# Kernel tuning notes

Hardware: AMD Instinct MI355X
Metric: run time of the kernel (lower is better)

The kernel has to match this reference:

```python
import jax, jax.numpy as jnp
import numpy as np

B, T, N, F_IN, F_OUT, K = 16, 12, 1024, 64, 64, 3


def setup_inputs() -> dict:
    key = jax.random.key(0)
    k1, k2, k3, k4 = jax.random.split(key, 4)
    x = jax.random.normal(k1, (B, T, N, F_IN), dtype=jnp.float32)
    spatial_attention = jax.random.uniform(k2, (B, N, N), dtype=jnp.float32)
    cheb = jax.random.normal(k3, (K, N, N), dtype=jnp.float32) / np.sqrt(N)
    # Xavier-uniform-ish init for Theta [K, F_in, F_out]
    limit = np.sqrt(6.0 / (F_IN + F_OUT))
    Theta = jax.random.uniform(k4, (K, F_IN, F_OUT), dtype=jnp.float32,
                               minval=-limit, maxval=limit)
    return {"x": x, "spatial_attention": spatial_attention, "cheb": cheb, "Theta": Theta}


def reference(x, spatial_attention, cheb, Theta):
    # Attention-weighted Chebyshev adjacencies: [B, K, N, N]
    A = cheb[None, :, :, :] * spatial_attention[:, None, :, :]
    # Graph propagation for all t, k at once: [B, T, K, N, F_in]
    rhs = jnp.einsum('bkij,btjf->btkif', A, x)
    # Per-order linear map + sum over K: [B, T, N, F_out]
    out = jnp.einsum('btkif,kfo->btio', rhs, Theta)
    return jax.nn.relu(out)
```

## Files before the change

### kernel.cpp

```cpp
#include <hip/hip_runtime.h>
#include <hip/hip_bf16.h>

#define BB 16
#define TT 12
#define NN 1024
#define FF 64
#define KC 3

typedef __bf16  bf16x8 __attribute__((ext_vector_type(8)));
typedef float   f32x4  __attribute__((ext_vector_type(4)));
typedef float   f32x16 __attribute__((ext_vector_type(16)));
typedef unsigned short u16;

#define A_TILE 24576
#define MFMA_B(a, b, c) __builtin_amdgcn_mfma_f32_32x32x16_bf16(a, b, c, 0, 0, 0)

#define YF_BYTES 25165824ull
#define CB_BYTES 6291456ull

static __device__ __forceinline__ u16 f2bf(float v) {
    union { __bf16 b; u16 u; } c; c.b = (__bf16)v; return c.u;
}

__global__ __launch_bounds__(256) void x_to_yfrags(
    const float* __restrict__ x, u16* __restrict__ y)
{
    __shared__ char tl[64 * 128];
    const int tid = threadIdx.x;
    const int bt  = blockIdx.x >> 4;
    const int jt  = blockIdx.x & 15;
    const int f   = tid & 63;
    const int jr  = tid >> 6;

    const float* xp = x + ((size_t)bt * NN + jt * 64 + jr) * FF + f;
    #pragma unroll
    for (int stp = 0; stp < 16; ++stp) {
        int j = stp * 4 + jr;
        u16 h = f2bf(xp[stp * 4 * FF]);
        *reinterpret_cast<u16*>(tl + j * 128 + ((f * 2) ^ ((j & 7) << 4))) = h;
    }
    __syncthreads();

    u16* yo = y + ((size_t)bt * 16 + jt) * 4096;
    #pragma unroll
    for (int p = 0; p < 2; ++p) {
        int c  = tid + p * 256;
        int s  = c >> 6, fo = c & 63;
        int j0 = (s >> 1) * 16 + (s & 1) * 8;
        u16 h[8];
        #pragma unroll
        for (int e = 0; e < 8; ++e)
            h[e] = *reinterpret_cast<u16*>(tl + (j0 + e) * 128 + ((fo * 2) ^ (e << 4)));
        uint4 w;
        w.x = h[0] | ((unsigned)h[1] << 16);
        w.y = h[2] | ((unsigned)h[3] << 16);
        w.z = h[4] | ((unsigned)h[5] << 16);
        w.w = h[6] | ((unsigned)h[7] << 16);
        *reinterpret_cast<uint4*>(yo + (size_t)c * 8) = w;
    }
}

__global__ __launch_bounds__(256) void cheb_to_bf16(
    const float* __restrict__ c, u16* __restrict__ o)
{
    const size_t i = ((size_t)blockIdx.x * 256 + threadIdx.x) * 8;
    f32x4 a = *reinterpret_cast<const f32x4*>(c + i);
    f32x4 b = *reinterpret_cast<const f32x4*>(c + i + 4);
    u16 h[8];
    #pragma unroll
    for (int e = 0; e < 4; ++e) { h[e] = f2bf(a[e]); h[e + 4] = f2bf(b[e]); }
    uint4 w;
    w.x = h[0] | ((unsigned)h[1] << 16);
    w.y = h[2] | ((unsigned)h[3] << 16);
    w.z = h[4] | ((unsigned)h[5] << 16);
    w.w = h[6] | ((unsigned)h[7] << 16);
    *reinterpret_cast<uint4*>(o + i) = w;
}

__global__ __launch_bounds__(512, 1) void cheb_main(
    const u16*  __restrict__ yfr,
    const float* __restrict__ att,
    const u16*  __restrict__ chb,
    const float* __restrict__ Theta,
    float* __restrict__ out)
{
    __shared__ __align__(16) char lds[2 * A_TILE];
    char* Ab0 = lds;
    char* Ab1 = lds + A_TILE;

    const int tid  = threadIdx.x;
    const int lane = tid & 63;
    const int wid  = tid >> 6;

    const int wg = (blockIdx.x & 7) * 96 + (blockIdx.x >> 3);
    const int b  = wg / 48;
    const int it = (wg % 48) / 3;
    const int tc = wg % 3;
    const int i_base = it * 64;
    const int t_base = tc * 4;

    const int wm  = wid >> 1;
    const int wn  = wid & 1;
    const int l31 = lane & 31;
    const int lg  = lane >> 5;
    const int sw3 = (l31 >> 2) & 7;

    const int r_a = tid >> 3;
    const int g_a = tid & 7;
    const int swza_st = ((r_a >> 2) & 7) << 4;
    const float* attR = att + ((size_t)b * NN + i_base + r_a) * NN + g_a * 8;
    const u16*   chR  = chb + ((size_t)(i_base + r_a)) * NN + g_a * 8;

    const u16* yt0 = yfr + ((size_t)(b * TT + t_base + wm) * 16) * 4096
                   + (size_t)(lg * 512 + l31 * 8);

    f32x16 acc[KC][2] = {};
    const int arow = (wn * 32 + l31) * 128;

    f32x4 ra0, ra1;
    bf16x8 rc[KC];
    bf16x8 y0[8], y1[8];

    auto LOADS = [&](int j0) {
        ra0 = *reinterpret_cast<const f32x4*>(attR + j0);
        ra1 = *reinterpret_cast<const f32x4*>(attR + j0 + 4);
        #pragma unroll
        for (int k = 0; k < KC; ++k)
            rc[k] = *reinterpret_cast<const bf16x8*>(chR + (size_t)k * NN * NN + j0);
    };
    auto FINISH = [&](char* Ab) {
        #pragma unroll
        for (int k = 0; k < KC; ++k) {
            bf16x8 w;
            #pragma unroll
            for (int e = 0; e < 4; ++e) {
                w[e]     = (__bf16)(ra0[e] * (float)rc[k][e]);
                w[e + 4] = (__bf16)(ra1[e] * (float)rc[k][e + 4]);
            }
            *reinterpret_cast<bf16x8*>(
                Ab + (k * 64 + r_a) * 128 + ((g_a * 16) ^ swza_st)) = w;
        }
    };
    auto loadY = [&](bf16x8* yd, int jt) {
        const u16* yt = yt0 + (size_t)jt * 4096;
        #pragma unroll
        for (int q = 0; q < 4; ++q) {
            yd[q * 2]     = *reinterpret_cast<const bf16x8*>(yt + q * 1024);
            yd[q * 2 + 1] = *reinterpret_cast<const bf16x8*>(yt + q * 1024 + 256);
        }
    };

    auto phase = [&](const char* AbR, bf16x8 af0, bf16x8 af1, int kk) {
        const int off = ((kk * 2 + lg) ^ sw3) << 4;
        bf16x8 b0 = *reinterpret_cast<const bf16x8*>(AbR + arow + off);
        bf16x8 b1 = *reinterpret_cast<const bf16x8*>(AbR + 8192 + arow + off);
        bf16x8 b2 = *reinterpret_cast<const bf16x8*>(AbR + 16384 + arow + off);
        __builtin_amdgcn_s_setprio(1);
        acc[0][0] = MFMA_B(af0, b0, acc[0][0]); acc[0][1] = MFMA_B(af1, b0, acc[0][1]);
        acc[1][0] = MFMA_B(af0, b1, acc[1][0]); acc[1][1] = MFMA_B(af1, b1, acc[1][1]);
        acc[2][0] = MFMA_B(af0, b2, acc[2][0]); acc[2][1] = MFMA_B(af1, b2, acc[2][1]);
        __builtin_amdgcn_s_setprio(0);
    };

    auto body = [&](char* curAb, char* altAb, bf16x8* yC, bf16x8* yN, int jt) {
        loadY(yN, (jt + 1) & 15);
        phase(curAb, yC[0], yC[1], 0);
        phase(curAb, yC[2], yC[3], 1);
        phase(curAb, yC[4], yC[5], 2);
        phase(curAb, yC[6], yC[7], 3);
        if (jt < 15) {
            FINISH(altAb);
            LOADS(((jt + 2) & 15) * 64);
        }
        asm volatile("s_waitcnt lgkmcnt(0)" ::: "memory");
        __builtin_amdgcn_s_barrier();
    };

    LOADS(0);
    loadY(y0, 0);
    FINISH(Ab0);
    LOADS(64);
    asm volatile("s_waitcnt lgkmcnt(0)" ::: "memory");
    __builtin_amdgcn_s_barrier();

    #pragma unroll 1
    for (int jt2 = 0; jt2 < 8; ++jt2) {
        body(Ab0, Ab1, y0, y1, jt2 * 2);
        body(Ab1, Ab0, y1, y0, jt2 * 2 + 1);
    }

    {
        const int fi0 = wid * 3;
        #pragma unroll
        for (int q = 0; q < 3; ++q) {
            int fi = fi0 + q;
            int k  = fi >> 3;
            int mo = (fi >> 2) & 1;
            int s  = fi & 3;
            int o  = 32 * mo + l31;
            int fb = 32 * (s >> 1) + 16 * (s & 1) + 4 * lg;
            bf16x8 v;
            #pragma unroll
            for (int e = 0; e < 8; ++e) {
                int f = fb + (e & 3) + 8 * (e >> 2);
                v[e] = (__bf16)Theta[(k * FF + f) * FF + o];
            }
            *reinterpret_cast<bf16x8*>(lds + (fi * 64 + lane) * 16) = v;
        }
    }
    __syncthreads();

    f32x16 of[2] = {};
    #pragma unroll
    for (int k = 0; k < KC; ++k) {
        #pragma unroll
        for (int s = 0; s < 4; ++s) {
            bf16x8 pb;
            #pragma unroll
            for (int e = 0; e < 8; ++e)
                pb[e] = (__bf16)acc[k][s >> 1][e + 8 * (s & 1)];
            #pragma unroll
            for (int mo = 0; mo < 2; ++mo) {
                bf16x8 th = *reinterpret_cast<const bf16x8*>(
                    lds + ((((k * 2 + mo) * 4 + s) * 64) + lane) * 16);
                of[mo] = MFMA_B(pb, th, of[mo]);
            }
        }
    }

    const int t = t_base + wm;
    float* op = out + (((size_t)b * TT + t) * NN + i_base + wn * 32) * FF;
    #pragma unroll
    for (int mo = 0; mo < 2; ++mo) {
        #pragma unroll
        for (int r = 0; r < 16; ++r) {
            int row = (r & 3) + 8 * (r >> 2) + 4 * lg;
            int o   = 32 * mo + l31;
            float v = of[mo][r];
            op[(size_t)row * FF + o] = v > 0.0f ? v : 0.0f;
        }
    }
}

__global__ __launch_bounds__(512, 2) void cheb_fused(
    const float* __restrict__ x, const float* __restrict__ att,
    const float* __restrict__ cheb, const float* __restrict__ Theta,
    float* __restrict__ out)
{
    __shared__ __align__(16) char lds_raw[2 * (A_TILE + 32768)];
    char* Ab0 = lds_raw;
    char* Xb0 = lds_raw + A_TILE;
    char* Ab1 = lds_raw + A_TILE + 32768;
    char* Xb1 = Ab1 + A_TILE;

    const int tid  = threadIdx.x;
    const int lane = tid & 63;
    const int wid  = tid >> 6;
    const int wg = (blockIdx.x & 7) * 96 + (blockIdx.x >> 3);
    const int b  = wg / 48;
    const int it = (wg % 48) / 3;
    const int tc = wg % 3;
    const int i_base = it * 64;
    const int t_base = tc * 4;
    const int wm  = wid >> 1;
    const int wn  = wid & 1;
    const int l31 = lane & 31;
    const int lg  = lane >> 5;
    const int sw3 = (l31 >> 2) & 7;
    const float* attB = att + (size_t)b * NN * NN;
    const float* xB   = x + (size_t)b * TT * NN * FF;
    const int r_a = tid >> 3;
    const int g_a = tid & 7;
    const int swza_st = ((r_a >> 2) & 7) << 4;
    int tl_s[4], jj_s[4], f_s[4], swzx_st[4];
    #pragma unroll
    for (int s = 0; s < 4; ++s) {
        int u = tid + s * 512;
        tl_s[s] = u >> 9;
        int rem = u & 511;
        jj_s[s] = (rem >> 4) * 2;
        f_s[s]  = (rem & 15) * 4;
        swzx_st[s] = ((f_s[s] >> 2) & 7) << 4;
    }
    f32x4 ra0, ra1, rc0[KC], rc1[KC], rx0[4], rx1[4];
    auto load_tile = [&](int j0) {
        const float* ap = attB + (size_t)(i_base + r_a) * NN + j0 + g_a * 8;
        ra0 = *reinterpret_cast<const f32x4*>(ap);
        ra1 = *reinterpret_cast<const f32x4*>(ap + 4);
        #pragma unroll
        for (int k = 0; k < KC; ++k) {
            const float* cp = cheb + ((size_t)k * NN + i_base + r_a) * NN + j0 + g_a * 8;
            rc0[k] = *reinterpret_cast<const f32x4*>(cp);
            rc1[k] = *reinterpret_cast<const f32x4*>(cp + 4);
        }
        #pragma unroll
        for (int s = 0; s < 4; ++s) {
            const float* xp = xB + ((size_t)(t_base + tl_s[s]) * NN + j0 + jj_s[s]) * FF + f_s[s];
            rx0[s] = *reinterpret_cast<const f32x4*>(xp);
            rx1[s] = *reinterpret_cast<const f32x4*>(xp + FF);
        }
    };
    auto store_A = [&](char* Ab) {
        #pragma unroll
        for (int k = 0; k < KC; ++k) {
            bf16x8 w;
            #pragma unroll
            for (int e = 0; e < 4; ++e) {
                w[e]     = (__bf16)(rc0[k][e] * ra0[e]);
                w[e + 4] = (__bf16)(rc1[k][e] * ra1[e]);
            }
            *reinterpret_cast<bf16x8*>(Ab + (k * 64 + r_a) * 128 + ((g_a * 16) ^ swza_st)) = w;
        }
    };
    auto store_X = [&](char* Xb) {
        #pragma unroll
        for (int s = 0; s < 4; ++s) {
            const int c0 = tl_s[s] * 64 + f_s[s];
            const int coloff = (jj_s[s] * 2) ^ swzx_st[s];
            #pragma unroll
            for (int e = 0; e < 4; ++e) {
                union { __bf16 h[2]; unsigned u32; } pk;
                pk.h[0] = (__bf16)rx0[s][e];
                pk.h[1] = (__bf16)rx1[s][e];
                *reinterpret_cast<unsigned*>(Xb + (c0 + e) * 128 + coloff) = pk.u32;
            }
        }
    };
    f32x16 acc[KC][2] = {};
    const int xrow0 = (wm * 64 + l31) * 128;
    const int xrow1 = xrow0 + 32 * 128;
    const int arow  = (wn * 32 + l31) * 128;
    auto phase = [&](const char* AbR, const char* XbR, int kk) {
        const int off = ((kk * 2 + lg) ^ sw3) << 4;
        bf16x8 af0 = *reinterpret_cast<const bf16x8*>(XbR + xrow0 + off);
        bf16x8 af1 = *reinterpret_cast<const bf16x8*>(XbR + xrow1 + off);
        bf16x8 b0  = *reinterpret_cast<const bf16x8*>(AbR + arow + off);
        bf16x8 b1  = *reinterpret_cast<const bf16x8*>(AbR + 8192 + arow + off);
        bf16x8 b2  = *reinterpret_cast<const bf16x8*>(AbR + 16384 + arow + off);
        __builtin_amdgcn_s_setprio(1);
        acc[0][0] = MFMA_B(af0, b0, acc[0][0]); acc[0][1] = MFMA_B(af1, b0, acc[0][1]);
        acc[1][0] = MFMA_B(af0, b1, acc[1][0]); acc[1][1] = MFMA_B(af1, b1, acc[1][1]);
        acc[2][0] = MFMA_B(af0, b2, acc[2][0]); acc[2][1] = MFMA_B(af1, b2, acc[2][1]);
        __builtin_amdgcn_s_setprio(0);
    };
    load_tile(0);
    store_A(Ab0);
    store_X(Xb0);
    load_tile(64);
    asm volatile("s_waitcnt lgkmcnt(0)" ::: "memory");
    __builtin_amdgcn_s_barrier();
    for (int jt2 = 0; jt2 < 8; ++jt2) {
        const int jt = jt2 * 2;
        phase(Ab0, Xb0, 0);
        phase(Ab0, Xb0, 1);
        store_A(Ab1);
        phase(Ab0, Xb0, 2);
        store_X(Xb1);
        phase(Ab0, Xb0, 3);
        if (jt + 2 < 16) load_tile((jt + 2) * 64);
        asm volatile("s_waitcnt lgkmcnt(0)" ::: "memory");
        __builtin_amdgcn_s_barrier();
        phase(Ab1, Xb1, 0);
        phase(Ab1, Xb1, 1);
        if (jt + 1 < 15) store_A(Ab0);
        phase(Ab1, Xb1, 2);
        if (jt + 1 < 15) store_X(Xb0);
        phase(Ab1, Xb1, 3);
        if (jt + 3 < 16) load_tile((jt + 3) * 64);
        asm volatile("s_waitcnt lgkmcnt(0)" ::: "memory");
        __builtin_amdgcn_s_barrier();
    }
    {
        const int fi0 = wid * 3;
        #pragma unroll
        for (int q = 0; q < 3; ++q) {
            int fi = fi0 + q;
            int k  = fi >> 3;
            int mo = (fi >> 2) & 1;
            int s  = fi & 3;
            int o  = 32 * mo + l31;
            int fb = 32 * (s >> 1) + 16 * (s & 1) + 4 * lg;
            bf16x8 v;
            #pragma unroll
            for (int e = 0; e < 8; ++e) {
                int f = fb + (e & 3) + 8 * (e >> 2);
                v[e] = (__bf16)Theta[(k * FF + f) * FF + o];
            }
            *reinterpret_cast<bf16x8*>(lds_raw + (fi * 64 + lane) * 16) = v;
        }
    }
    __syncthreads();
    f32x16 of[2] = {};
    #pragma unroll
    for (int k = 0; k < KC; ++k) {
        #pragma unroll
        for (int s = 0; s < 4; ++s) {
            bf16x8 pb;
            #pragma unroll
            for (int e = 0; e < 8; ++e)
                pb[e] = (__bf16)acc[k][s >> 1][e + 8 * (s & 1)];
            #pragma unroll
            for (int mo = 0; mo < 2; ++mo) {
                bf16x8 th = *reinterpret_cast<const bf16x8*>(
                    lds_raw + ((((k * 2 + mo) * 4 + s) * 64) + lane) * 16);
                of[mo] = MFMA_B(pb, th, of[mo]);
            }
        }
    }
    const int t = t_base + wm;
    float* op = out + (((size_t)b * TT + t) * NN + i_base + wn * 32) * FF;
    #pragma unroll
    for (int mo = 0; mo < 2; ++mo) {
        #pragma unroll
        for (int r = 0; r < 16; ++r) {
            int row = (r & 3) + 8 * (r >> 2) + 4 * lg;
            int o   = 32 * mo + l31;
            float v = of[mo][r];
            op[(size_t)row * FF + o] = v > 0.0f ? v : 0.0f;
        }
    }
}

extern "C" void kernel_launch(void* const* d_in, const int* in_sizes, int n_in,
                              void* d_out, int out_size, void* d_ws, size_t ws_size,
                              hipStream_t stream) {
    const float* x     = (const float*)d_in[0];
    const float* att   = (const float*)d_in[1];
    const float* cheb  = (const float*)d_in[2];
    const float* Theta = (const float*)d_in[3];
    float* out = (float*)d_out;
    (void)in_sizes; (void)n_in; (void)out_size;

    if (ws_size >= YF_BYTES + CB_BYTES) {
        u16* yfr = (u16*)d_ws;
        u16* cbf = (u16*)((char*)d_ws + YF_BYTES);
        x_to_yfrags<<<dim3(BB * TT * 16), 256, 0, stream>>>(x, yfr);
        cheb_to_bf16<<<dim3(KC * NN * NN / (256 * 8)), 256, 0, stream>>>(cheb, cbf);
        cheb_main<<<dim3(BB * 16 * 3), 512, 0, stream>>>(yfr, att, cbf, Theta, out);
    } else {
        cheb_fused<<<dim3(BB * 16 * 3), 512, 0, stream>>>(x, att, cheb, Theta, out);
    }
}
```

Baseline: 108.7 us.

## Process two j-tiles per barrier interval with paired LDS buffers

Doubles LDS to hold two A tiles per buffer, so each barrier interval computes two j-tiles and builds the next pair. This halves the number of workgroup barriers and moves the A-tile construction (FINISH/LOADS) ahead of the MFMA phases to overlap global loads with compute. In exchange, LDS use grows to 96KB and register pressure rises. The last iterations also build tiles that wrap around modulo 16 and are never used.

```diff
diff --git a/kernel.cpp b/kernel.cpp
--- a/kernel.cpp
+++ b/kernel.cpp
@@ -13,6 +13,7 @@
 typedef unsigned short u16;
 
 #define A_TILE 24576
+#define A_PAIR (2 * A_TILE)
 #define MFMA_B(a, b, c) __builtin_amdgcn_mfma_f32_32x32x16_bf16(a, b, c, 0, 0, 0)
 
 #define YF_BYTES 25165824ull
@@ -84,9 +85,9 @@
     const float* __restrict__ Theta,
     float* __restrict__ out)
 {
-    __shared__ __align__(16) char lds[2 * A_TILE];
+    __shared__ __align__(16) char lds[2 * A_PAIR];
     char* Ab0 = lds;
-    char* Ab1 = lds + A_TILE;
+    char* Ab1 = lds + A_PAIR;
 
     const int tid  = threadIdx.x;
     const int lane = tid & 63;
@@ -150,43 +151,50 @@
         }
     };
 
-    auto phase = [&](const char* AbR, bf16x8 af0, bf16x8 af1, int kk) {
-        const int off = ((kk * 2 + lg) ^ sw3) << 4;
-        bf16x8 b0 = *reinterpret_cast<const bf16x8*>(AbR + arow + off);
-        bf16x8 b1 = *reinterpret_cast<const bf16x8*>(AbR + 8192 + arow + off);
-        bf16x8 b2 = *reinterpret_cast<const bf16x8*>(AbR + 16384 + arow + off);
-        __builtin_amdgcn_s_setprio(1);
-        acc[0][0] = MFMA_B(af0, b0, acc[0][0]); acc[0][1] = MFMA_B(af1, b0, acc[0][1]);
-        acc[1][0] = MFMA_B(af0, b1, acc[1][0]); acc[1][1] = MFMA_B(af1, b1, acc[1][1]);
-        acc[2][0] = MFMA_B(af0, b2, acc[2][0]); acc[2][1] = MFMA_B(af1, b2, acc[2][1]);
-        __builtin_amdgcn_s_setprio(0);
-    };
-
-    auto body = [&](char* curAb, char* altAb, bf16x8* yC, bf16x8* yN, int jt) {
-        loadY(yN, (jt + 1) & 15);
-        phase(curAb, yC[0], yC[1], 0);
-        phase(curAb, yC[2], yC[3], 1);
-        phase(curAb, yC[4], yC[5], 2);
-        phase(curAb, yC[6], yC[7], 3);
-        if (jt < 15) {
-            FINISH(altAb);
-            LOADS(((jt + 2) & 15) * 64);
-        }
+    auto phase4 = [&](const char* Abase, const bf16x8* yv) {
+        #pragma unroll
+        for (int kk = 0; kk < 4; ++kk) {
+            const int off = ((kk * 2 + lg) ^ sw3) << 4;
+            bf16x8 af0 = yv[kk * 2];
+            bf16x8 af1 = yv[kk * 2 + 1];
+            bf16x8 b0 = *reinterpret_cast<const bf16x8*>(Abase + arow + off);
+            bf16x8 b1 = *reinterpret_cast<const bf16x8*>(Abase + 8192 + arow + off);
+            bf16x8 b2 = *reinterpret_cast<const bf16x8*>(Abase + 16384 + arow + off);
+            __builtin_amdgcn_s_setprio(1);
+            acc[0][0] = MFMA_B(af0, b0, acc[0][0]); acc[0][1] = MFMA_B(af1, b0, acc[0][1]);
+            acc[1][0] = MFMA_B(af0, b1, acc[1][0]); acc[1][1] = MFMA_B(af1, b1, acc[1][1]);
+            acc[2][0] = MFMA_B(af0, b2, acc[2][0]); acc[2][1] = MFMA_B(af1, b2, acc[2][1]);
+            __builtin_amdgcn_s_setprio(0);
+        }
+    };
+
+    auto interval = [&](char* cur, char* alt, int p) {
+        loadY(y1, (p + 1) & 15);
+        FINISH(alt);
+        LOADS(((p + 3) & 15) * 64);
+        phase4(cur, y0);
+        loadY(y0, (p + 2) & 15);
+        FINISH(alt + A_TILE);
+        LOADS(((p + 4) & 15) * 64);
+        phase4(cur + A_TILE, y1);
         asm volatile("s_waitcnt lgkmcnt(0)" ::: "memory");
         __builtin_amdgcn_s_barrier();
     };
 
     LOADS(0);
-    loadY(y0, 0);
     FINISH(Ab0);
     LOADS(64);
+    FINISH(Ab0 + A_TILE);
+    LOADS(128);
+    loadY(y0, 0);
     asm volatile("s_waitcnt lgkmcnt(0)" ::: "memory");
     __builtin_amdgcn_s_barrier();
 
     #pragma unroll 1
-    for (int jt2 = 0; jt2 < 8; ++jt2) {
-        body(Ab0, Ab1, y0, y1, jt2 * 2);
-        body(Ab1, Ab0, y1, y0, jt2 * 2 + 1);
+    for (int h = 0; h < 8; ++h) {
+        char* cur = (h & 1) ? Ab1 : Ab0;
+        char* alt = (h & 1) ? Ab0 : Ab1;
+        interval(cur, alt, 2 * h);
     }
 
     {
```

After: 121.2 us. 1.11x slower.

## Stage Y fragments through double-buffered LDS via direct global-to-LDS loads

Applied to the files above, without the earlier changes.

Y operand fragments are no longer prefetched into per-wave register arrays. Each block now loads them once into a double-buffered LDS region with global_load_lds, and every wave reads them from LDS inside the MFMA loop. This removes the duplicate global loads made by waves that share the same Y rows, and frees the 64 VGPRs the y0/y1 arrays used. In exchange it adds LDS reads per k-step, grows shared memory to about 112KB, and depends on a hand-written vmcnt(5) wait for correct ordering.

```diff
diff --git a/kernel.cpp b/kernel.cpp
--- a/kernel.cpp
+++ b/kernel.cpp
@@ -13,6 +13,7 @@
 typedef unsigned short u16;
 
 #define A_TILE 24576
+#define Y_TILE 32768
 #define MFMA_B(a, b, c) __builtin_amdgcn_mfma_f32_32x32x16_bf16(a, b, c, 0, 0, 0)
 
 #define YF_BYTES 25165824ull
@@ -20,6 +21,12 @@
 
 static __device__ __forceinline__ u16 f2bf(float v) {
     union { __bf16 b; u16 u; } c; c.b = (__bf16)v; return c.u;
+}
+
+static __device__ __forceinline__ void load_lds16(const void* g, void* l) {
+    __builtin_amdgcn_global_load_lds(
+        (const __attribute__((address_space(1))) unsigned int*)g,
+        (__attribute__((address_space(3))) unsigned int*)l, 16, 0, 0);
 }
 
 __global__ __launch_bounds__(256) void x_to_yfrags(
@@ -84,9 +91,11 @@
     const float* __restrict__ Theta,
     float* __restrict__ out)
 {
-    __shared__ __align__(16) char lds[2 * A_TILE];
+    __shared__ __align__(16) char lds[2 * A_TILE + 2 * Y_TILE];
     char* Ab0 = lds;
     char* Ab1 = lds + A_TILE;
+    char* Yb0 = lds + 2 * A_TILE;
+    char* Yb1 = Yb0 + Y_TILE;
 
     const int tid  = threadIdx.x;
     const int lane = tid & 63;
@@ -111,15 +120,11 @@
     const float* attR = att + ((size_t)b * NN + i_base + r_a) * NN + g_a * 8;
     const u16*   chR  = chb + ((size_t)(i_base + r_a)) * NN + g_a * 8;
 
-    const u16* yt0 = yfr + ((size_t)(b * TT + t_base + wm) * 16) * 4096
-                   + (size_t)(lg * 512 + l31 * 8);
-
     f32x16 acc[KC][2] = {};
     const int arow = (wn * 32 + l31) * 128;
 
     f32x4 ra0, ra1;
     bf16x8 rc[KC];
-    bf16x8 y0[8], y1[8];
 
     auto LOADS = [&](int j0) {
         ra0 = *reinterpret_cast<const f32x4*>(attR + j0);
@@ -141,52 +146,63 @@
                 Ab + (k * 64 + r_a) * 128 + ((g_a * 16) ^ swza_st)) = w;
         }
     };
-    auto loadY = [&](bf16x8* yd, int jt) {
-        const u16* yt = yt0 + (size_t)jt * 4096;
+
+    auto loadY_lds = [&](char* Yb, int jt) {
         #pragma unroll
         for (int q = 0; q < 4; ++q) {
-            yd[q * 2]     = *reinterpret_cast<const bf16x8*>(yt + q * 1024);
-            yd[q * 2 + 1] = *reinterpret_cast<const bf16x8*>(yt + q * 1024 + 256);
-        }
-    };
-
-    auto phase = [&](const char* AbR, bf16x8 af0, bf16x8 af1, int kk) {
-        const int off = ((kk * 2 + lg) ^ sw3) << 4;
-        bf16x8 b0 = *reinterpret_cast<const bf16x8*>(AbR + arow + off);
-        bf16x8 b1 = *reinterpret_cast<const bf16x8*>(AbR + 8192 + arow + off);
-        bf16x8 b2 = *reinterpret_cast<const bf16x8*>(AbR + 16384 + arow + off);
-        __builtin_amdgcn_s_setprio(1);
-        acc[0][0] = MFMA_B(af0, b0, acc[0][0]); acc[0][1] = MFMA_B(af1, b0, acc[0][1]);
-        acc[1][0] = MFMA_B(af0, b1, acc[1][0]); acc[1][1] = MFMA_B(af1, b1, acc[1][1]);
-        acc[2][0] = MFMA_B(af0, b2, acc[2][0]); acc[2][1] = MFMA_B(af1, b2, acc[2][1]);
-        __builtin_amdgcn_s_setprio(0);
-    };
-
-    auto body = [&](char* curAb, char* altAb, bf16x8* yC, bf16x8* yN, int jt) {
-        loadY(yN, (jt + 1) & 15);
-        phase(curAb, yC[0], yC[1], 0);
-        phase(curAb, yC[2], yC[3], 1);
-        phase(curAb, yC[4], yC[5], 2);
-        phase(curAb, yC[6], yC[7], 3);
+            int s    = wid * 4 + q;
+            int tile = s >> 3;
+            int part = s & 7;
+            const u16* gp = yfr + ((size_t)(b * TT + t_base + tile) * 16 + jt) * 4096
+                          + (size_t)(part * 64 + lane) * 8;
+            load_lds16(gp, Yb + tile * 8192 + part * 1024);
+        }
+    };
+
+    auto phase4 = [&](const char* Abase, const char* Ybase) {
+        const char* yt = Ybase + wm * 8192;
+        #pragma unroll
+        for (int kk = 0; kk < 4; ++kk) {
+            const int off  = ((kk * 2 + lg) ^ sw3) << 4;
+            const int yoff = (kk * 2 + lg) * 1024 + l31 * 16;
+            bf16x8 af0 = *reinterpret_cast<const bf16x8*>(yt + yoff);
+            bf16x8 af1 = *reinterpret_cast<const bf16x8*>(yt + yoff + 512);
+            bf16x8 b0 = *reinterpret_cast<const bf16x8*>(Abase + arow + off);
+            bf16x8 b1 = *reinterpret_cast<const bf16x8*>(Abase + 8192 + arow + off);
+            bf16x8 b2 = *reinterpret_cast<const bf16x8*>(Abase + 16384 + arow + off);
+            __builtin_amdgcn_s_setprio(1);
+            acc[0][0] = MFMA_B(af0, b0, acc[0][0]); acc[0][1] = MFMA_B(af1, b0, acc[0][1]);
+            acc[1][0] = MFMA_B(af0, b1, acc[1][0]); acc[1][1] = MFMA_B(af1, b1, acc[1][1]);
+            acc[2][0] = MFMA_B(af0, b2, acc[2][0]); acc[2][1] = MFMA_B(af1, b2, acc[2][1]);
+            __builtin_amdgcn_s_setprio(0);
+        }
+    };
+
+    auto body = [&](char* curA, char* altA, char* curY, char* altY, int jt) {
+        loadY_lds(altY, (jt + 1) & 15);
+        __builtin_amdgcn_sched_barrier(0);
+        phase4(curA, curY);
         if (jt < 15) {
-            FINISH(altAb);
+            FINISH(altA);
             LOADS(((jt + 2) & 15) * 64);
         }
+        asm volatile("s_waitcnt vmcnt(5)" ::: "memory");
         asm volatile("s_waitcnt lgkmcnt(0)" ::: "memory");
         __builtin_amdgcn_s_barrier();
     };
 
+    loadY_lds(Yb0, 0);
     LOADS(0);
-    loadY(y0, 0);
+    asm volatile("s_waitcnt vmcnt(0)" ::: "memory");
     FINISH(Ab0);
     LOADS(64);
     asm volatile("s_waitcnt lgkmcnt(0)" ::: "memory");
     __builtin_amdgcn_s_barrier();
 
     #pragma unroll 1
-    for (int jt2 = 0; jt2 < 8; ++jt2) {
-        body(Ab0, Ab1, y0, y1, jt2 * 2);
-        body(Ab1, Ab0, y1, y0, jt2 * 2 + 1);
+    for (int h = 0; h < 8; ++h) {
+        body(Ab0, Ab1, Yb0, Yb1, 2 * h);
+        body(Ab1, Ab0, Yb1, Yb0, 2 * h + 1);
     }
 
     {
```

After: 105.9 us. 1.03x faster.
